# Kernel tuning notes

Hardware: AMD Instinct MI355X
Metric: run time of the kernel (lower is better)

## Reference

```python
import jax, jax.numpy as jnp
import numpy as np

N, T, D, H, W = 2, 1024, 1024, 16, 64  # batch, seq, embed, heads, temporal_window
DH = D // H                             # head_dim = 64
WIN = 2 * W + 1                         # 129


def setup_inputs() -> dict:
    key = jax.random.key(0)
    ks = jax.random.split(key, 10)
    s = 0.02
    inp = {"x": jax.random.normal(ks[0], (N, T, D), jnp.float32)}
    inp["w_q"] = jax.random.normal(ks[1], (D, D), jnp.float32) * s
    inp["b_q"] = jnp.zeros((D,), jnp.float32)
    inp["w_k"] = jax.random.normal(ks[2], (D, D), jnp.float32) * s
    inp["b_k"] = jnp.zeros((D,), jnp.float32)
    inp["w_v"] = jax.random.normal(ks[3], (D, D), jnp.float32) * s
    inp["b_v"] = jnp.zeros((D,), jnp.float32)
    inp["w_o"] = jax.random.normal(ks[4], (D, D), jnp.float32) * s
    inp["b_o"] = jnp.zeros((D,), jnp.float32)
    return inp


def reference(x, w_q, b_q, w_k, b_k, w_v, b_v, w_o, b_o):
    # x: (N, T, D). Windowed MHA: query t attends to positions [t-W, t+W].
    n, t_len, d = x.shape
    scale = 1.0 / jnp.sqrt(jnp.asarray(DH, x.dtype))

    q = (x @ w_q.T + b_q).reshape(n, t_len, H, DH)
    k = (x @ w_k.T + b_k).reshape(n, t_len, H, DH)
    v = (x @ w_v.T + b_v).reshape(n, t_len, H, DH)

    # window index map: pos[t, r] = t + r - W  (r in [0, 2W])
    t_idx = jnp.arange(t_len)[:, None]
    r_idx = jnp.arange(WIN)[None, :]
    pos = t_idx + r_idx - W
    valid = (pos >= 0) & (pos < t_len)
    idx = jnp.clip(pos, 0, t_len - 1)

    k_win = k[:, idx]
    v_win = v[:, idx]

    scores = jnp.einsum('nthd,ntwhd->nhtw', q, k_win) * scale
    scores = jnp.where(valid[None, None], scores, -jnp.inf)
    p = jax.nn.softmax(scores, axis=-1)

    out = jnp.einsum('nhtw,ntwhd->nthd', p, v_win).reshape(n, t_len, d)
    return out @ w_o.T + b_o
```

## Files before the change

### kernel.cpp

```cpp
#include <hip/hip_runtime.h>
#include <hip/hip_fp16.h>
#include <cstdint>
#include <cstddef>

using f16x8 = _Float16 __attribute__((ext_vector_type(8)));
using f16x4 = _Float16 __attribute__((ext_vector_type(4)));
using f32x4 = float __attribute__((ext_vector_type(4)));

#define GLDS16(g, l) __builtin_amdgcn_global_load_lds(                        \
    (const __attribute__((address_space(1))) void*)(g),                       \
    (__attribute__((address_space(3))) void*)(l), 16, 0, 0)

__device__ inline void cast4(const float* __restrict__ in,
                             _Float16* __restrict__ out, int i) {
  float4 v = reinterpret_cast<const float4*>(in)[i];
  f16x4 h;
  h[0] = (_Float16)v.x; h[1] = (_Float16)v.y;
  h[2] = (_Float16)v.z; h[3] = (_Float16)v.w;
  reinterpret_cast<f16x4*>(out)[i] = h;
}

__global__ void prep_kernel(const float* __restrict__ x,
                            const float* __restrict__ wq, const float* __restrict__ wk,
                            const float* __restrict__ wv, const float* __restrict__ wo,
                            const float* __restrict__ bq, const float* __restrict__ bk,
                            const float* __restrict__ bv,
                            _Float16* __restrict__ xh, _Float16* __restrict__ wcat,
                            _Float16* __restrict__ woh, float* __restrict__ bcat) {
  int i = blockIdx.x * blockDim.x + threadIdx.x;
  const int XU = 512 * 1024;
  const int WU = 256 * 1024;
  if (i < XU) { cast4(x, xh, i); return; }
  i -= XU;
  if (i < WU) { cast4(wq, wcat, i); return; }
  i -= WU;
  if (i < WU) { cast4(wk, wcat + 1024 * 1024, i); return; }
  i -= WU;
  if (i < WU) { cast4(wv, wcat + 2 * 1024 * 1024, i); return; }
  i -= WU;
  if (i < WU) { cast4(wo, woh, i); return; }
  i -= WU;
  if (i < 256) { reinterpret_cast<float4*>(bcat)[i] = reinterpret_cast<const float4*>(bq)[i]; return; }
  i -= 256;
  if (i < 256) { reinterpret_cast<float4*>(bcat + 1024)[i] = reinterpret_cast<const float4*>(bk)[i]; return; }
  i -= 256;
  if (i < 256) { reinterpret_cast<float4*>(bcat + 2048)[i] = reinterpret_cast<const float4*>(bv)[i]; return; }
}

template <int BM, typename TOUT>
__global__ __launch_bounds__(256) void gemm_bt(
    const _Float16* __restrict__ A, const _Float16* __restrict__ B,
    const float* __restrict__ bias, TOUT* __restrict__ C,
    int M, int N, int K) {
  constexpr int WM = BM / 2;
  constexpr int MI = WM / 16;
  __shared__ _Float16 As[BM * 32];
  __shared__ _Float16 Bs[128 * 32];

  const int tid  = threadIdx.x;
  const int lane = tid & 63;
  const int wave = tid >> 6;
  const int l15  = lane & 15;
  const int quad = lane >> 4;
  const int m0 = blockIdx.y * BM;
  const int n0 = blockIdx.x * 128;
  const int wr = (wave >> 1) * WM;
  const int wc = (wave & 1) * 64;

  const int srow = tid >> 2;
  const int skc  = (tid & 3) * 8;
  const _Float16* Ag0 = A + (size_t)(m0 + srow) * K + skc;
  const _Float16* Ag1 = A + (size_t)(m0 + 64 + srow) * K + skc;
  const _Float16* Bg0 = B + (size_t)(n0 + srow) * K + skc;
  const _Float16* Bg1 = B + (size_t)(n0 + 64 + srow) * K + skc;
  _Float16* Asd0 = &As[tid * 8];
  _Float16* Asd1 = &As[(256 + tid) * 8];
  _Float16* Bsd0 = &Bs[tid * 8];
  _Float16* Bsd1 = &Bs[(256 + tid) * 8];

  f32x4 acc[MI][4];
#pragma unroll
  for (int i = 0; i < MI; i++)
#pragma unroll
    for (int j = 0; j < 4; j++) acc[i][j] = f32x4{0.f, 0.f, 0.f, 0.f};

  for (int kt = 0; kt < K; kt += 32) {
    __syncthreads();
    GLDS16(Ag0 + kt, Asd0);
    if constexpr (BM == 128) GLDS16(Ag1 + kt, Asd1);
    GLDS16(Bg0 + kt, Bsd0);
    GLDS16(Bg1 + kt, Bsd1);
    __syncthreads();

    f16x8 af[MI], bf[4];
#pragma unroll
    for (int mi = 0; mi < MI; mi++)
      af[mi] = *reinterpret_cast<const f16x8*>(&As[(wr + mi * 16 + l15) * 32 + quad * 8]);
#pragma unroll
    for (int ni = 0; ni < 4; ni++)
      bf[ni] = *reinterpret_cast<const f16x8*>(&Bs[(wc + ni * 16 + l15) * 32 + quad * 8]);
#pragma unroll
    for (int mi = 0; mi < MI; mi++)
#pragma unroll
      for (int ni = 0; ni < 4; ni++)
        acc[mi][ni] = __builtin_amdgcn_mfma_f32_16x16x32_f16(af[mi], bf[ni], acc[mi][ni], 0, 0, 0);
  }

#pragma unroll
  for (int mi = 0; mi < MI; mi++) {
    const int row = m0 + wr + mi * 16 + quad * 4;
#pragma unroll
    for (int ni = 0; ni < 4; ni++) {
      const int col = n0 + wc + ni * 16 + l15;
      const float bv = bias ? bias[col] : 0.f;
#pragma unroll
      for (int r = 0; r < 4; r++) {
        float v = acc[mi][ni][r] + bv;
        C[(size_t)(row + r) * N + col] = (TOUT)v;
      }
    }
  }
}

#define T_LEN 1024
#define KSTR 72
#define VSTR 200

__global__ __launch_bounds__(256) void attn_win(
    const _Float16* __restrict__ qkv, _Float16* __restrict__ o) {
  __shared__ _Float16 KP[192 * KSTR];
  __shared__ _Float16 Vt[64 * VSTR];

  const int b  = blockIdx.x;
  const int qt = b & 15;
  const int h  = (b >> 4) & 15;
  const int n  = b >> 8;
  const int t0 = qt * 64;

  const int tid  = threadIdx.x;
  const int lane = tid & 63;
  const int wave = tid >> 6;
  const int l15  = lane & 15;
  const int quad = lane >> 4;

  const size_t rowstr = 3072;
  const _Float16* qbase = qkv + (size_t)n * T_LEN * rowstr + h * 64;
  const _Float16* kbase = qbase + 1024;
  const _Float16* vbase = qbase + 2048;

  for (int idx = tid; idx < 192 * 8; idx += 256) {
    const int j  = idx >> 3;
    const int d8 = (idx & 7) * 8;
    const int t  = t0 - 64 + j;
    f16x8 kv;
    if (t >= 0 && t < T_LEN) {
      kv = *reinterpret_cast<const f16x8*>(kbase + (size_t)t * rowstr + d8);
    } else {
      for (int i = 0; i < 8; i++) kv[i] = (_Float16)0.f;
    }
    *reinterpret_cast<f16x8*>(&KP[j * KSTR + d8]) = kv;
  }
  for (int it = 0; it < 6; it++) {
    const int item = it * 256 + tid;
    const int j    = (item & 63) + ((item >> 9) << 6);
    const int dgrp = (item >> 6) & 7;
    const int t = t0 - 64 + j;
    f16x8 vv;
    if (t >= 0 && t < T_LEN) {
      vv = *reinterpret_cast<const f16x8*>(vbase + (size_t)t * rowstr + dgrp * 8);
    } else {
      for (int i = 0; i < 8; i++) vv[i] = (_Float16)0.f;
    }
#pragma unroll
    for (int i = 0; i < 8; i++) Vt[(dgrp * 8 + i) * VSTR + j] = vv[i];
  }
  __syncthreads();

  const _Float16* qrow = qbase + (size_t)(t0 + wave * 16 + l15) * rowstr;
  const f16x8 qf0 = *reinterpret_cast<const f16x8*>(qrow + quad * 8);
  const f16x8 qf1 = *reinterpret_cast<const f16x8*>(qrow + 32 + quad * 8);

  f32x4 accs[12];
#pragma unroll
  for (int jt = 0; jt < 12; jt++) accs[jt] = f32x4{0.f, 0.f, 0.f, 0.f};
#pragma unroll
  for (int jt = 0; jt < 12; jt++) {
    const f16x8 b0 = *reinterpret_cast<const f16x8*>(&KP[(jt * 16 + l15) * KSTR + quad * 8]);
    const f16x8 b1 = *reinterpret_cast<const f16x8*>(&KP[(jt * 16 + l15) * KSTR + 32 + quad * 8]);
    accs[jt] = __builtin_amdgcn_mfma_f32_16x16x32_f16(qf0, b0, accs[jt], 0, 0, 0);
    accs[jt] = __builtin_amdgcn_mfma_f32_16x16x32_f16(qf1, b1, accs[jt], 0, 0, 0);
  }
  __syncthreads();

  float rmax[4] = {-1e30f, -1e30f, -1e30f, -1e30f};
#pragma unroll
  for (int jt = 0; jt < 12; jt++) {
    const int jcol = jt * 16 + l15;
    const int tabs = t0 - 64 + jcol;
#pragma unroll
    for (int r = 0; r < 4; r++) {
      const int q = wave * 16 + quad * 4 + r;
      const bool valid = (jcol >= q) && (jcol <= q + 128) && (tabs >= 0) && (tabs < T_LEN);
      const float s = valid ? accs[jt][r] * 0.125f : -1e30f;
      accs[jt][r] = s;
      rmax[r] = fmaxf(rmax[r], s);
    }
  }
#pragma unroll
  for (int r = 0; r < 4; r++)
#pragma unroll
    for (int m = 1; m < 16; m <<= 1) rmax[r] = fmaxf(rmax[r], __shfl_xor(rmax[r], m));

  float rsum[4] = {0.f, 0.f, 0.f, 0.f};
#pragma unroll
  for (int jt = 0; jt < 12; jt++)
#pragma unroll
    for (int r = 0; r < 4; r++) {
      const float p = __expf(accs[jt][r] - rmax[r]);
      accs[jt][r] = p;
      rsum[r] += p;
    }
#pragma unroll
  for (int r = 0; r < 4; r++)
#pragma unroll
    for (int m = 1; m < 16; m <<= 1) rsum[r] += __shfl_xor(rsum[r], m);

  _Float16* Pw = &KP[wave * 16 * VSTR];
#pragma unroll
  for (int jt = 0; jt < 12; jt++)
#pragma unroll
    for (int r = 0; r < 4; r++)
      Pw[(quad * 4 + r) * VSTR + jt * 16 + l15] = (_Float16)accs[jt][r];
  __syncthreads();

  f32x4 acco[4];
#pragma unroll
  for (int ni = 0; ni < 4; ni++) acco[ni] = f32x4{0.f, 0.f, 0.f, 0.f};
#pragma unroll
  for (int ks = 0; ks < 6; ks++) {
    const f16x8 pa = *reinterpret_cast<const f16x8*>(&Pw[l15 * VSTR + ks * 32 + quad * 8]);
#pragma unroll
    for (int ni = 0; ni < 4; ni++) {
      const f16x8 vb = *reinterpret_cast<const f16x8*>(&Vt[(ni * 16 + l15) * VSTR + ks * 32 + quad * 8]);
      acco[ni] = __builtin_amdgcn_mfma_f32_16x16x32_f16(pa, vb, acco[ni], 0, 0, 0);
    }
  }

  float rinv[4];
#pragma unroll
  for (int r = 0; r < 4; r++) rinv[r] = 1.f / rsum[r];

  _Float16* obase = o + (size_t)(n * T_LEN + t0 + wave * 16) * 1024 + h * 64;
#pragma unroll
  for (int ni = 0; ni < 4; ni++)
#pragma unroll
    for (int r = 0; r < 4; r++)
      obase[(size_t)(quad * 4 + r) * 1024 + ni * 16 + l15] = (_Float16)(acco[ni][r] * rinv[r]);
}

extern "C" void kernel_launch(void* const* d_in, const int* in_sizes, int n_in,
                              void* d_out, int out_size, void* d_ws, size_t ws_size,
                              hipStream_t stream) {
  const float* x   = (const float*)d_in[0];
  const float* w_q = (const float*)d_in[1];
  const float* b_q = (const float*)d_in[2];
  const float* w_k = (const float*)d_in[3];
  const float* b_k = (const float*)d_in[4];
  const float* w_v = (const float*)d_in[5];
  const float* b_v = (const float*)d_in[6];
  const float* w_o = (const float*)d_in[7];
  const float* b_o = (const float*)d_in[8];
  float* out = (float*)d_out;

  char* ws = (char*)d_ws;
  _Float16* xh   = (_Float16*)(ws);
  _Float16* wcat = (_Float16*)(ws + (4ull << 20));
  _Float16* woh  = (_Float16*)(ws + (10ull << 20));
  _Float16* qkvh = (_Float16*)(ws + (12ull << 20));
  _Float16* oh   = xh;
  float*    bcat = (float*)(ws + (24ull << 20));

  const int PREP_UNITS = 512 * 1024 + 4 * 256 * 1024 + 3 * 256;
  prep_kernel<<<(PREP_UNITS + 255) / 256, 256, 0, stream>>>(
      x, w_q, w_k, w_v, w_o, b_q, b_k, b_v, xh, wcat, woh, bcat);

  gemm_bt<128, _Float16><<<dim3(24, 16), 256, 0, stream>>>(xh, wcat, bcat, qkvh, 2048, 3072, 1024);

  attn_win<<<512, 256, 0, stream>>>(qkvh, oh);

  gemm_bt<64, float><<<dim3(8, 32), 256, 0, stream>>>(oh, woh, b_o, out, 2048, 1024, 1024);
}
```

Before: 147.0 us.

## Double-buffer GEMM LDS tiles, remap blocks across XCDs, hoist Q loads

The GEMM now keeps two LDS buffers and issues the global-to-LDS loads for the next K tile before computing on the current one. This lets memory latency overlap with MFMA work and removes one barrier per iteration. Block indices are remapped so that consecutive N tiles land on the same XCD, which should improve L2 reuse of the A tiles. In the attention kernel, the Q fragment loads are moved ahead of the K/V staging loop so their latency is hidden. The cost is double the LDS per block, which may lower occupancy. The remap also assumes gridDim.x is divisible by 8.

```diff
diff --git a/kernel.cpp b/kernel.cpp
--- a/kernel.cpp
+++ b/kernel.cpp
@@ -54,16 +54,24 @@
     int M, int N, int K) {
   constexpr int WM = BM / 2;
   constexpr int MI = WM / 16;
-  __shared__ _Float16 As[BM * 32];
-  __shared__ _Float16 Bs[128 * 32];
+  __shared__ _Float16 As[2][BM * 32];
+  __shared__ _Float16 Bs[2][128 * 32];
 
   const int tid  = threadIdx.x;
   const int lane = tid & 63;
   const int wave = tid >> 6;
   const int l15  = lane & 15;
   const int quad = lane >> 4;
-  const int m0 = blockIdx.y * BM;
-  const int n0 = blockIdx.x * 128;
+
+  const int nlin = blockIdx.y * gridDim.x + blockIdx.x;
+  const int xcd  = nlin & 7;
+  const int slot = nlin >> 3;
+  const int cpx  = gridDim.x >> 3;
+  const int bx   = xcd * cpx + (slot % cpx);
+  const int by   = slot / cpx;
+
+  const int m0 = by * BM;
+  const int n0 = bx * 128;
   const int wr = (wave >> 1) * WM;
   const int wc = (wave & 1) * 64;
 
@@ -73,10 +81,6 @@
   const _Float16* Ag1 = A + (size_t)(m0 + 64 + srow) * K + skc;
   const _Float16* Bg0 = B + (size_t)(n0 + srow) * K + skc;
   const _Float16* Bg1 = B + (size_t)(n0 + 64 + srow) * K + skc;
-  _Float16* Asd0 = &As[tid * 8];
-  _Float16* Asd1 = &As[(256 + tid) * 8];
-  _Float16* Bsd0 = &Bs[tid * 8];
-  _Float16* Bsd1 = &Bs[(256 + tid) * 8];
 
   f32x4 acc[MI][4];
 #pragma unroll
@@ -84,27 +88,37 @@
 #pragma unroll
     for (int j = 0; j < 4; j++) acc[i][j] = f32x4{0.f, 0.f, 0.f, 0.f};
 
-  for (int kt = 0; kt < K; kt += 32) {
-    __syncthreads();
-    GLDS16(Ag0 + kt, Asd0);
-    if constexpr (BM == 128) GLDS16(Ag1 + kt, Asd1);
-    GLDS16(Bg0 + kt, Bsd0);
-    GLDS16(Bg1 + kt, Bsd1);
-    __syncthreads();
-
+  auto prefetch = [&](int kt, int buf) {
+    GLDS16(Ag0 + kt, &As[buf][tid * 8]);
+    if constexpr (BM == 128) GLDS16(Ag1 + kt, &As[buf][(256 + tid) * 8]);
+    GLDS16(Bg0 + kt, &Bs[buf][tid * 8]);
+    GLDS16(Bg1 + kt, &Bs[buf][(256 + tid) * 8]);
+  };
+  auto compute = [&](int buf) {
     f16x8 af[MI], bf[4];
 #pragma unroll
     for (int mi = 0; mi < MI; mi++)
-      af[mi] = *reinterpret_cast<const f16x8*>(&As[(wr + mi * 16 + l15) * 32 + quad * 8]);
+      af[mi] = *reinterpret_cast<const f16x8*>(&As[buf][(wr + mi * 16 + l15) * 32 + quad * 8]);
 #pragma unroll
     for (int ni = 0; ni < 4; ni++)
-      bf[ni] = *reinterpret_cast<const f16x8*>(&Bs[(wc + ni * 16 + l15) * 32 + quad * 8]);
+      bf[ni] = *reinterpret_cast<const f16x8*>(&Bs[buf][(wc + ni * 16 + l15) * 32 + quad * 8]);
 #pragma unroll
     for (int mi = 0; mi < MI; mi++)
 #pragma unroll
       for (int ni = 0; ni < 4; ni++)
         acc[mi][ni] = __builtin_amdgcn_mfma_f32_16x16x32_f16(af[mi], bf[ni], acc[mi][ni], 0, 0, 0);
-  }
+  };
+
+  const int NI = K >> 5;
+  prefetch(0, 0);
+  __syncthreads();
+#pragma unroll 2
+  for (int i = 0; i < NI - 1; ++i) {
+    prefetch((i + 1) << 5, (i + 1) & 1);
+    compute(i & 1);
+    __syncthreads();
+  }
+  compute((NI - 1) & 1);
 
 #pragma unroll
   for (int mi = 0; mi < MI; mi++) {
@@ -147,6 +161,10 @@
   const _Float16* qbase = qkv + (size_t)n * T_LEN * rowstr + h * 64;
   const _Float16* kbase = qbase + 1024;
   const _Float16* vbase = qbase + 2048;
+
+  const _Float16* qrow = qbase + (size_t)(t0 + wave * 16 + l15) * rowstr;
+  const f16x8 qf0 = *reinterpret_cast<const f16x8*>(qrow + quad * 8);
+  const f16x8 qf1 = *reinterpret_cast<const f16x8*>(qrow + 32 + quad * 8);
 
   for (int idx = tid; idx < 192 * 8; idx += 256) {
     const int j  = idx >> 3;
@@ -175,10 +193,6 @@
     for (int i = 0; i < 8; i++) Vt[(dgrp * 8 + i) * VSTR + j] = vv[i];
   }
   __syncthreads();
-
-  const _Float16* qrow = qbase + (size_t)(t0 + wave * 16 + l15) * rowstr;
-  const f16x8 qf0 = *reinterpret_cast<const f16x8*>(qrow + quad * 8);
-  const f16x8 qf1 = *reinterpret_cast<const f16x8*>(qrow + 32 + quad * 8);
 
   f32x4 accs[12];
 #pragma unroll
```

Result: no change. 146.9 us (-0.0%).

## Use 32x32 MFMA tiles in GEMM, XCD-aware block remap, hoist Q loads

Applied to the files above, without the earlier changes.

The GEMM kernel switches from 16x16x32 to 32x32x16 MFMA instructions, so each wave computes larger output tiles with fewer LDS fragment loads per FLOP. It also remaps block indices so that consecutive blocks landing on the same XCD share N-column panels for better L2 reuse, and adds a launch_bounds occupancy hint of 4 blocks. In the attention kernel the Q fragment loads are moved ahead of the K/V staging so their global latency overlaps with it. The XCD remap assumes gridDim.x is divisible by 8, and the 32x32 output layout writes scattered rows in the epilogue.

```diff
diff --git a/kernel.cpp b/kernel.cpp
--- a/kernel.cpp
+++ b/kernel.cpp
@@ -3,9 +3,10 @@
 #include <cstdint>
 #include <cstddef>
 
-using f16x8 = _Float16 __attribute__((ext_vector_type(8)));
-using f16x4 = _Float16 __attribute__((ext_vector_type(4)));
-using f32x4 = float __attribute__((ext_vector_type(4)));
+using f16x8  = _Float16 __attribute__((ext_vector_type(8)));
+using f16x4  = _Float16 __attribute__((ext_vector_type(4)));
+using f32x4  = float __attribute__((ext_vector_type(4)));
+using f32x16 = float __attribute__((ext_vector_type(16)));
 
 #define GLDS16(g, l) __builtin_amdgcn_global_load_lds(                        \
     (const __attribute__((address_space(1))) void*)(g),                       \
@@ -48,22 +49,30 @@
 }
 
 template <int BM, typename TOUT>
-__global__ __launch_bounds__(256) void gemm_bt(
+__global__ __launch_bounds__(256, 4) void gemm_bt(
     const _Float16* __restrict__ A, const _Float16* __restrict__ B,
     const float* __restrict__ bias, TOUT* __restrict__ C,
     int M, int N, int K) {
   constexpr int WM = BM / 2;
-  constexpr int MI = WM / 16;
+  constexpr int MI = WM / 32;
   __shared__ _Float16 As[BM * 32];
   __shared__ _Float16 Bs[128 * 32];
 
   const int tid  = threadIdx.x;
   const int lane = tid & 63;
   const int wave = tid >> 6;
-  const int l15  = lane & 15;
-  const int quad = lane >> 4;
-  const int m0 = blockIdx.y * BM;
-  const int n0 = blockIdx.x * 128;
+  const int l31  = lane & 31;
+  const int half = lane >> 5;
+
+  const int nlin = blockIdx.y * gridDim.x + blockIdx.x;
+  const int xcd  = nlin & 7;
+  const int slot = nlin >> 3;
+  const int cpx  = gridDim.x >> 3;
+  const int bx   = xcd * cpx + (slot % cpx);
+  const int by   = slot / cpx;
+
+  const int m0 = by * BM;
+  const int n0 = bx * 128;
   const int wr = (wave >> 1) * WM;
   const int wc = (wave & 1) * 64;
 
@@ -73,50 +82,51 @@
   const _Float16* Ag1 = A + (size_t)(m0 + 64 + srow) * K + skc;
   const _Float16* Bg0 = B + (size_t)(n0 + srow) * K + skc;
   const _Float16* Bg1 = B + (size_t)(n0 + 64 + srow) * K + skc;
-  _Float16* Asd0 = &As[tid * 8];
-  _Float16* Asd1 = &As[(256 + tid) * 8];
-  _Float16* Bsd0 = &Bs[tid * 8];
-  _Float16* Bsd1 = &Bs[(256 + tid) * 8];
-
-  f32x4 acc[MI][4];
+
+  f32x16 acc[MI][2];
 #pragma unroll
   for (int i = 0; i < MI; i++)
 #pragma unroll
-    for (int j = 0; j < 4; j++) acc[i][j] = f32x4{0.f, 0.f, 0.f, 0.f};
+    for (int j = 0; j < 2; j++) acc[i][j] = (f32x16)0.0f;
 
   for (int kt = 0; kt < K; kt += 32) {
     __syncthreads();
-    GLDS16(Ag0 + kt, Asd0);
-    if constexpr (BM == 128) GLDS16(Ag1 + kt, Asd1);
-    GLDS16(Bg0 + kt, Bsd0);
-    GLDS16(Bg1 + kt, Bsd1);
+    GLDS16(Ag0 + kt, &As[tid * 8]);
+    if constexpr (BM == 128) GLDS16(Ag1 + kt, &As[(256 + tid) * 8]);
+    GLDS16(Bg0 + kt, &Bs[tid * 8]);
+    GLDS16(Bg1 + kt, &Bs[(256 + tid) * 8]);
     __syncthreads();
 
-    f16x8 af[MI], bf[4];
-#pragma unroll
-    for (int mi = 0; mi < MI; mi++)
-      af[mi] = *reinterpret_cast<const f16x8*>(&As[(wr + mi * 16 + l15) * 32 + quad * 8]);
-#pragma unroll
-    for (int ni = 0; ni < 4; ni++)
-      bf[ni] = *reinterpret_cast<const f16x8*>(&Bs[(wc + ni * 16 + l15) * 32 + quad * 8]);
-#pragma unroll
-    for (int mi = 0; mi < MI; mi++)
-#pragma unroll
-      for (int ni = 0; ni < 4; ni++)
-        acc[mi][ni] = __builtin_amdgcn_mfma_f32_16x16x32_f16(af[mi], bf[ni], acc[mi][ni], 0, 0, 0);
+#pragma unroll
+    for (int kh = 0; kh < 2; kh++) {
+      f16x8 af[MI], bf[2];
+#pragma unroll
+      for (int mi = 0; mi < MI; mi++)
+        af[mi] = *reinterpret_cast<const f16x8*>(
+            &As[(wr + mi * 32 + l31) * 32 + kh * 16 + half * 8]);
+#pragma unroll
+      for (int ni = 0; ni < 2; ni++)
+        bf[ni] = *reinterpret_cast<const f16x8*>(
+            &Bs[(wc + ni * 32 + l31) * 32 + kh * 16 + half * 8]);
+#pragma unroll
+      for (int mi = 0; mi < MI; mi++)
+#pragma unroll
+        for (int ni = 0; ni < 2; ni++)
+          acc[mi][ni] = __builtin_amdgcn_mfma_f32_32x32x16_f16(af[mi], bf[ni], acc[mi][ni], 0, 0, 0);
+    }
   }
 
 #pragma unroll
   for (int mi = 0; mi < MI; mi++) {
-    const int row = m0 + wr + mi * 16 + quad * 4;
-#pragma unroll
-    for (int ni = 0; ni < 4; ni++) {
-      const int col = n0 + wc + ni * 16 + l15;
+    const int rbase = m0 + wr + mi * 32 + 4 * half;
+#pragma unroll
+    for (int ni = 0; ni < 2; ni++) {
+      const int col = n0 + wc + ni * 32 + l31;
       const float bv = bias ? bias[col] : 0.f;
 #pragma unroll
-      for (int r = 0; r < 4; r++) {
-        float v = acc[mi][ni][r] + bv;
-        C[(size_t)(row + r) * N + col] = (TOUT)v;
+      for (int r = 0; r < 16; r++) {
+        const int row = rbase + (r & 3) + 8 * (r >> 2);
+        C[(size_t)row * N + col] = (TOUT)(acc[mi][ni][r] + bv);
       }
     }
   }
@@ -147,6 +157,10 @@
   const _Float16* qbase = qkv + (size_t)n * T_LEN * rowstr + h * 64;
   const _Float16* kbase = qbase + 1024;
   const _Float16* vbase = qbase + 2048;
+
+  const _Float16* qrow = qbase + (size_t)(t0 + wave * 16 + l15) * rowstr;
+  const f16x8 qf0 = *reinterpret_cast<const f16x8*>(qrow + quad * 8);
+  const f16x8 qf1 = *reinterpret_cast<const f16x8*>(qrow + 32 + quad * 8);
 
   for (int idx = tid; idx < 192 * 8; idx += 256) {
     const int j  = idx >> 3;
@@ -175,10 +189,6 @@
     for (int i = 0; i < 8; i++) Vt[(dgrp * 8 + i) * VSTR + j] = vv[i];
   }
   __syncthreads();
-
-  const _Float16* qrow = qbase + (size_t)(t0 + wave * 16 + l15) * rowstr;
-  const f16x8 qf0 = *reinterpret_cast<const f16x8*>(qrow + quad * 8);
-  const f16x8 qf1 = *reinterpret_cast<const f16x8*>(qrow + 32 + quad * 8);
 
   f32x4 accs[12];
 #pragma unroll
```

Result: no change. 146.2 us (-0.5%).
